# Performance work log

Measured on AMD Instinct MI355X. Metric: run time of the kernel, lower is better.

Reference implementation:

```python
import jax, jax.numpy as jnp
import numpy as np

DIM = 256
NUM_HEADS = 4
HEAD_DIM = DIM // NUM_HEADS
SCALE = HEAD_DIM ** -0.5


def setup_inputs() -> dict:
    key = jax.random.key(0)
    k1, k2, k3, k4 = jax.random.split(key, 4)
    B, N, C = 2, 4096, DIM
    x = jax.random.normal(k1, (B, N, C), dtype=jnp.float32)
    # nn.Linear(dim, 3*dim, bias=False): weight [3C, C], y = x @ W.T
    w_qkv = jax.random.normal(k2, (3 * C, C), dtype=jnp.float32) * (C ** -0.5)
    # nn.Linear(dim, dim) with bias
    w_proj = jax.random.normal(k3, (C, C), dtype=jnp.float32) * (C ** -0.5)
    b_proj = jax.random.normal(k4, (C,), dtype=jnp.float32) * 0.02
    return {"x": x, "w_qkv": w_qkv, "w_proj": w_proj, "b_proj": b_proj}


def reference(x, w_qkv, w_proj, b_proj):
    B, N, C = x.shape
    H, D = NUM_HEADS, HEAD_DIM
    qkv = x @ w_qkv.T                                  # [B, N, 3C]
    qkv = qkv.reshape(B, N, 3, H, D).transpose(2, 0, 3, 1, 4)  # [3, B, H, N, D]
    q, k, v = qkv[0], qkv[1], qkv[2]
    attn = jnp.einsum("bhnd,bhmd->bhnm", q, k) * SCALE  # [B, H, N, N]
    attn = jax.nn.softmax(attn, axis=-1)
    out = jnp.einsum("bhnm,bhmd->bhnd", attn, v)        # [B, H, N, D]
    out = out.transpose(0, 2, 1, 3).reshape(B, N, C)
    out = out @ w_proj.T + b_proj
    return out
```

## Files before the change

kernel.cpp:

```cpp
#include <hip/hip_runtime.h>
#include <hip/hip_bf16.h>
#include <stdint.h>

typedef __bf16 bf16;
typedef __bf16 bf16x8 __attribute__((ext_vector_type(8)));
typedef __bf16 bf16x4 __attribute__((ext_vector_type(4)));
typedef float  f32x4  __attribute__((ext_vector_type(4)));

#define MFMA16(a, b, c) __builtin_amdgcn_mfma_f32_16x16x32_bf16((a), (b), (c), 0, 0, 0)

#define BB   2
#define NN   4096
#define CC   256
#define HH   4
#define DD   64
#define BH   8
#define SL2E 0.1803368801111244f

__device__ __forceinline__ void gload_lds16(const void* g, void* l) {
    __builtin_amdgcn_global_load_lds(
        (const __attribute__((address_space(1))) void*)g,
        (__attribute__((address_space(3))) void*)l, 16, 0, 0);
}

__global__ __launch_bounds__(256) void cvt_all(const float* __restrict__ x,
                                               const float* __restrict__ wq,
                                               const float* __restrict__ wp,
                                               bf16* __restrict__ xb,
                                               bf16* __restrict__ wqb,
                                               bf16* __restrict__ wpb) {
    int i = blockIdx.x * 256 + threadIdx.x;
    const float* src; bf16* dst; int j;
    if (i < 524288)      { src = x;  dst = xb;  j = i; }
    else if (i < 573440) { src = wq; dst = wqb; j = i - 524288; }
    else if (i < 589824) { src = wp; dst = wpb; j = i - 573440; }
    else return;
    f32x4 v = ((const f32x4*)src)[j];
    bf16x4 o;
    o[0] = (bf16)v[0]; o[1] = (bf16)v[1]; o[2] = (bf16)v[2]; o[3] = (bf16)v[3];
    ((bf16x4*)dst)[j] = o;
}

__global__ __launch_bounds__(256) void gemm_qkv(const bf16* __restrict__ X,
                                                const bf16* __restrict__ W,
                                                bf16* __restrict__ Q,
                                                bf16* __restrict__ K,
                                                bf16* __restrict__ Vt) {
    const int wave = threadIdx.x >> 6;
    const int lane = threadIdx.x & 63;
    const int lr = lane & 15;
    const int lg = lane >> 4;
    const int row0 = blockIdx.x * 128 + wave * 32;
    const int col0 = blockIdx.y * 64;

    f32x4 acc[2][4] = {};
    for (int k0 = 0; k0 < 256; k0 += 32) {
        bf16x8 a[2], b[4];
#pragma unroll
        for (int i = 0; i < 2; i++)
            a[i] = *(const bf16x8*)&X[(size_t)(row0 + 16 * i + lr) * 256 + k0 + 8 * lg];
#pragma unroll
        for (int t = 0; t < 4; t++)
            b[t] = *(const bf16x8*)&W[(size_t)(col0 + 16 * t + lr) * 256 + k0 + 8 * lg];
#pragma unroll
        for (int i = 0; i < 2; i++)
#pragma unroll
            for (int t = 0; t < 4; t++)
                acc[i][t] = MFMA16(a[i], b[t], acc[i][t]);
    }

    const int s = col0 >> 8;
    const int h = (col0 >> 6) & 3;
    if (s == 2) {
#pragma unroll
        for (int i = 0; i < 2; i++) {
#pragma unroll
            for (int t = 0; t < 4; t++) {
                int row = row0 + 16 * i + 4 * lg;
                int d   = 16 * t + lr;
                int bh  = ((row >> 12) << 2) | h;
                int nb  = row & 4095;
                int g   = nb >> 5, m = (nb >> 2) & 7;
                int np  = (g << 5) + ((m & 3) << 3) + ((m >> 2) << 2);
                bf16x4 o4;
#pragma unroll
                for (int r = 0; r < 4; r++) o4[r] = (bf16)acc[i][t][r];
                *(bf16x4*)&Vt[((size_t)bh * DD + d) * NN + np] = o4;
            }
        }
    } else {
        bf16* dst = (s == 0) ? Q : K;
        const float sc = (s == 0) ? SL2E : 1.0f;
#pragma unroll
        for (int i = 0; i < 2; i++) {
#pragma unroll
            for (int t = 0; t < 4; t++) {
#pragma unroll
                for (int r = 0; r < 4; r++) {
                    int row = row0 + 16 * i + 4 * lg + r;
                    int d   = 16 * t + lr;
                    int bh  = ((row >> 12) << 2) | h;
                    int n   = row & 4095;
                    dst[((size_t)bh * NN + n) * DD + d] = (bf16)(acc[i][t][r] * sc);
                }
            }
        }
    }
}

template<int NSPLIT>
__global__ __launch_bounds__(256, 2) void flash_attn(const bf16* __restrict__ Q,
                                                     const bf16* __restrict__ K,
                                                     const bf16* __restrict__ Vt,
                                                     bf16* __restrict__ Op,
                                                     float* __restrict__ ps) {
    __shared__ __align__(16) char kv_lds[2][16384];

    const int id  = blockIdx.x + 16 * (blockIdx.y + 8 * blockIdx.z);
    constexpr int CHUNK = 16 * NSPLIT;
    const int nid = (id & 7) * CHUNK + (id >> 3);
    const int qx  = nid & 15;
    const int g   = nid >> 4;
    const int bh  = g & 7;
    const int zid = g >> 3;

    const int wave = threadIdx.x >> 6;
    const int lane = threadIdx.x & 63;
    const int lr   = lane & 15;
    const int lg   = lane >> 4;
    const int tid  = threadIdx.x;
    const int swz  = (lr & 7) << 4;

    const char* Khb  = (const char*)(K  + (size_t)bh * NN * DD);
    const char* Vthb = (const char*)(Vt + (size_t)bh * DD * NN);
    const bf16* Qh   = Q + (size_t)bh * NN * DD;

    const int qw = qx * 256 + wave * 64;

    bf16x8 qf[4][2];
#pragma unroll
    for (int s = 0; s < 4; s++) {
        qf[s][0] = *(const bf16x8*)&Qh[(size_t)(qw + 16 * s + lr) * DD + 8 * lg];
        qf[s][1] = *(const bf16x8*)&Qh[(size_t)(qw + 16 * s + lr) * DD + 32 + 8 * lg];
    }

    const int L  = tid * 16;
    const int r0 = L >> 7;
    const int c0 = (L & 127) ^ ((r0 & 7) << 4);

    bf16x8 onesf;
#pragma unroll
    for (int j = 0; j < 8; j++) onesf[j] = (bf16)1.0f;

    f32x4 oa[4][4] = {};
    f32x4 psacc[4] = {};

    auto stage = [&](int t, char* buf) {
        const int kv0 = t * 64;
        gload_lds16(Khb + (size_t)(kv0 + r0) * 128 + c0,             buf + L);
        gload_lds16(Khb + (size_t)(kv0 + r0 + 32) * 128 + c0,        buf + 4096 + L);
        gload_lds16(Vthb + (size_t)r0 * 8192 + kv0 * 2 + c0,         buf + 8192 + L);
        gload_lds16(Vthb + (size_t)(r0 + 32) * 8192 + kv0 * 2 + c0,  buf + 12288 + L);
    };

    auto compute = [&](const char* buf) {
        const char* kb = buf;
        const char* vb = buf + 8192;

        bf16x8 pb[4][2];
        __builtin_amdgcn_s_setprio(1);
#pragma unroll
        for (int t = 0; t < 4; t++) {
            const char* rowk = kb + (16 * t + lr) * 128;
            bf16x8 kf0 = *(const bf16x8*)(rowk + ((16 * lg) ^ swz));
            bf16x8 kf1 = *(const bf16x8*)(rowk + ((64 + 16 * lg) ^ swz));
#pragma unroll
            for (int s = 0; s < 4; s++) {
                f32x4 z = {0.f, 0.f, 0.f, 0.f};
                z = MFMA16(kf0, qf[s][0], z);
                z = MFMA16(kf1, qf[s][1], z);
#pragma unroll
                for (int r = 0; r < 4; r++)
                    pb[s][t >> 1][4 * (t & 1) + r] = (bf16)__builtin_exp2f(z[r]);
            }
        }
        __builtin_amdgcn_s_setprio(0);

        bf16x8 vf[2][4];
#pragma unroll
        for (int dt = 0; dt < 4; dt++) {
            const char* rowv = vb + (16 * dt + lr) * 128;
            vf[0][dt] = *(const bf16x8*)(rowv + ((16 * lg) ^ swz));
            vf[1][dt] = *(const bf16x8*)(rowv + ((64 + 16 * lg) ^ swz));
        }

        __builtin_amdgcn_s_setprio(1);
#pragma unroll
        for (int s = 0; s < 4; s++) {
#pragma unroll
            for (int dt = 0; dt < 4; dt++) {
                oa[s][dt] = MFMA16(vf[0][dt], pb[s][0], oa[s][dt]);
                oa[s][dt] = MFMA16(vf[1][dt], pb[s][1], oa[s][dt]);
            }
            psacc[s] = MFMA16(onesf, pb[s][0], psacc[s]);
            psacc[s] = MFMA16(onesf, pb[s][1], psacc[s]);
        }
        __builtin_amdgcn_s_setprio(0);
    };

    constexpr int nt = 64 / NSPLIT;
    const int t0 = zid * nt;

    char* cur = &kv_lds[0][0];
    char* nxt = &kv_lds[1][0];

    stage(t0, cur);
    stage(t0 + 1, nxt);

    for (int t = 0; t < nt; t++) {
        if (t + 1 < nt) asm volatile("s_waitcnt vmcnt(4)" ::: "memory");
        else            asm volatile("s_waitcnt vmcnt(0)" ::: "memory");
        __builtin_amdgcn_s_barrier();
        compute(cur);
        asm volatile("" ::: "memory");
        __builtin_amdgcn_s_barrier();
        if (t + 2 < nt) stage(t0 + t + 2, cur);
        char* tmp = cur; cur = nxt; nxt = tmp;
    }

    const int b = bh >> 2, hd = bh & 3;
#pragma unroll
    for (int s = 0; s < 4; s++) {
        const int q = qw + 16 * s + lr;
        bf16* Oz = Op + (size_t)zid * 8192 * 256
                      + ((size_t)b * NN + q) * CC + hd * 64;
#pragma unroll
        for (int dt = 0; dt < 4; dt++) {
            bf16x4 o4;
#pragma unroll
            for (int i = 0; i < 4; i++) o4[i] = (bf16)oa[s][dt][i];
            *(bf16x4*)&Oz[16 * dt + 4 * lg] = o4;
        }
        ps[((size_t)zid * BH + bh) * NN + q] = psacc[s][0];
    }
}

template<int NSPLIT>
__global__ __launch_bounds__(256) void gemm_proj(const bf16* __restrict__ Op,
                                                 const float* __restrict__ ps,
                                                 const bf16* __restrict__ W,
                                                 const float* __restrict__ bias,
                                                 float* __restrict__ Out) {
    const int wave = threadIdx.x >> 6;
    const int lane = threadIdx.x & 63;
    const int lr = lane & 15;
    const int lg = lane >> 4;
    const int row0 = blockIdx.x * 128 + wave * 32;
    const int col0 = blockIdx.y * 64;

    float rinv[2][4];
#pragma unroll
    for (int i = 0; i < 2; i++) {
        int row = row0 + 16 * i + lr;
        int n = row & 4095, b = row >> 12;
#pragma unroll
        for (int h = 0; h < 4; h++) {
            float s0 = 0.0f;
#pragma unroll
            for (int z = 0; z < NSPLIT; z++)
                s0 += ps[((size_t)z * BH + b * 4 + h) * NN + n];
            rinv[i][h] = 1.0f / s0;
        }
    }

    f32x4 acc[2][4] = {};
    for (int k0 = 0; k0 < 256; k0 += 32) {
        const int h = k0 >> 6;
        bf16x8 a[2], b4[4];
#pragma unroll
        for (int i = 0; i < 2; i++) {
            size_t base = (size_t)(row0 + 16 * i + lr) * 256 + k0 + 8 * lg;
            float av[8] = {};
#pragma unroll
            for (int z = 0; z < NSPLIT; z++) {
                bf16x8 u = *(const bf16x8*)&Op[base + (size_t)z * 8192 * 256];
#pragma unroll
                for (int j = 0; j < 8; j++) av[j] += (float)u[j];
            }
            const float rv = rinv[i][h];
#pragma unroll
            for (int j = 0; j < 8; j++) a[i][j] = (bf16)(av[j] * rv);
        }
#pragma unroll
        for (int t = 0; t < 4; t++)
            b4[t] = *(const bf16x8*)&W[(size_t)(col0 + 16 * t + lr) * 256 + k0 + 8 * lg];
#pragma unroll
        for (int i = 0; i < 2; i++)
#pragma unroll
            for (int t = 0; t < 4; t++)
                acc[i][t] = MFMA16(a[i], b4[t], acc[i][t]);
    }
#pragma unroll
    for (int t = 0; t < 4; t++) {
        float bv = bias[col0 + 16 * t + lr];
#pragma unroll
        for (int i = 0; i < 2; i++) {
#pragma unroll
            for (int r = 0; r < 4; r++) {
                int row = row0 + 16 * i + 4 * lg + r;
                Out[(size_t)row * 256 + col0 + 16 * t + lr] = acc[i][t][r] + bv;
            }
        }
    }
}

extern "C" void kernel_launch(void* const* d_in, const int* in_sizes, int n_in,
                              void* d_out, int out_size, void* d_ws, size_t ws_size,
                              hipStream_t stream) {
    const float* x      = (const float*)d_in[0];
    const float* w_qkv  = (const float*)d_in[1];
    const float* w_proj = (const float*)d_in[2];
    const float* b_proj = (const float*)d_in[3];
    float* out = (float*)d_out;

    char* ws = (char*)d_ws;
    size_t off = 0;
    auto alloc = [&](size_t bytes) { void* p = ws + off; off += (bytes + 255) & ~(size_t)255; return p; };

    bf16* xb  = (bf16*)alloc((size_t)8192 * 256 * 2);
    bf16* wqb = (bf16*)alloc((size_t)768 * 256 * 2);
    bf16* wpb = (bf16*)alloc((size_t)256 * 256 * 2);
    bf16* Qb  = (bf16*)alloc((size_t)BH * NN * DD * 2);
    bf16* Kb  = (bf16*)alloc((size_t)BH * NN * DD * 2);
    bf16* Vtb = (bf16*)alloc((size_t)BH * NN * DD * 2);

    const size_t opBytes = (size_t)8192 * 256 * 2;
    const size_t psBytes = (size_t)BH * NN * 4;
    const size_t perSplit = ((opBytes + 255) & ~(size_t)255) + ((psBytes + 255) & ~(size_t)255);
    const size_t rem = (ws_size > off) ? (ws_size - off) : 0;
    const int nsplit = (rem >= 4 * perSplit) ? 4 : ((rem >= 2 * perSplit) ? 2 : 1);

    bf16*  Op = (bf16*)alloc(opBytes * nsplit);
    float* ps = (float*)alloc(psBytes * nsplit);

    cvt_all<<<2304, 256, 0, stream>>>(x, w_qkv, w_proj, xb, wqb, wpb);
    gemm_qkv<<<dim3(64, 12), 256, 0, stream>>>(xb, wqb, Qb, Kb, Vtb);
    if (nsplit == 4) {
        flash_attn<4><<<dim3(16, 8, 4), 256, 0, stream>>>(Qb, Kb, Vtb, Op, ps);
        gemm_proj<4><<<dim3(64, 4), 256, 0, stream>>>(Op, ps, wpb, b_proj, out);
    } else if (nsplit == 2) {
        flash_attn<2><<<dim3(16, 8, 2), 256, 0, stream>>>(Qb, Kb, Vtb, Op, ps);
        gemm_proj<2><<<dim3(64, 4), 256, 0, stream>>>(Op, ps, wpb, b_proj, out);
    } else {
        flash_attn<1><<<dim3(16, 8, 1), 256, 0, stream>>>(Qb, Kb, Vtb, Op, ps);
        gemm_proj<1><<<dim3(64, 4), 256, 0, stream>>>(Op, ps, wpb, b_proj, out);
    }
}
```

Before: 101.0 us.

## Replace LDS-staged K/V pipeline with direct global loads in single-wave blocks

```diff
diff --git a/kernel.cpp b/kernel.cpp
--- a/kernel.cpp
+++ b/kernel.cpp
@@ -16,12 +16,6 @@
 #define DD   64
 #define BH   8
 #define SL2E 0.1803368801111244f
-
-__device__ __forceinline__ void gload_lds16(const void* g, void* l) {
-    __builtin_amdgcn_global_load_lds(
-        (const __attribute__((address_space(1))) void*)g,
-        (__attribute__((address_space(3))) void*)l, 16, 0, 0);
-}
 
 __global__ __launch_bounds__(256) void cvt_all(const float* __restrict__ x,
                                                const float* __restrict__ wq,
@@ -109,33 +103,29 @@
 }
 
 template<int NSPLIT>
-__global__ __launch_bounds__(256, 2) void flash_attn(const bf16* __restrict__ Q,
-                                                     const bf16* __restrict__ K,
-                                                     const bf16* __restrict__ Vt,
-                                                     bf16* __restrict__ Op,
-                                                     float* __restrict__ ps) {
-    __shared__ __align__(16) char kv_lds[2][16384];
-
-    const int id  = blockIdx.x + 16 * (blockIdx.y + 8 * blockIdx.z);
-    constexpr int CHUNK = 16 * NSPLIT;
+__global__ __launch_bounds__(64, 2) void flash_attn(const bf16* __restrict__ Q,
+                                                    const bf16* __restrict__ K,
+                                                    const bf16* __restrict__ Vt,
+                                                    bf16* __restrict__ Op,
+                                                    float* __restrict__ ps) {
+    constexpr int TOTAL = 64 * 8 * NSPLIT;
+    constexpr int CHUNK = TOTAL / 8;
+    const int id  = blockIdx.x + 64 * (blockIdx.y + 8 * blockIdx.z);
     const int nid = (id & 7) * CHUNK + (id >> 3);
-    const int qx  = nid & 15;
-    const int g   = nid >> 4;
+    const int qx  = nid & 63;
+    const int g   = nid >> 6;
     const int bh  = g & 7;
     const int zid = g >> 3;
 
-    const int wave = threadIdx.x >> 6;
     const int lane = threadIdx.x & 63;
     const int lr   = lane & 15;
     const int lg   = lane >> 4;
-    const int tid  = threadIdx.x;
-    const int swz  = (lr & 7) << 4;
 
     const char* Khb  = (const char*)(K  + (size_t)bh * NN * DD);
     const char* Vthb = (const char*)(Vt + (size_t)bh * DD * NN);
     const bf16* Qh   = Q + (size_t)bh * NN * DD;
 
-    const int qw = qx * 256 + wave * 64;
+    const int qw = qx * 64;
 
     bf16x8 qf[4][2];
 #pragma unroll
@@ -144,10 +134,6 @@
         qf[s][1] = *(const bf16x8*)&Qh[(size_t)(qw + 16 * s + lr) * DD + 32 + 8 * lg];
     }
 
-    const int L  = tid * 16;
-    const int r0 = L >> 7;
-    const int c0 = (L & 127) ^ ((r0 & 7) << 4);
-
     bf16x8 onesf;
 #pragma unroll
     for (int j = 0; j < 8; j++) onesf[j] = (bf16)1.0f;
@@ -155,77 +141,51 @@
     f32x4 oa[4][4] = {};
     f32x4 psacc[4] = {};
 
-    auto stage = [&](int t, char* buf) {
-        const int kv0 = t * 64;
-        gload_lds16(Khb + (size_t)(kv0 + r0) * 128 + c0,             buf + L);
-        gload_lds16(Khb + (size_t)(kv0 + r0 + 32) * 128 + c0,        buf + 4096 + L);
-        gload_lds16(Vthb + (size_t)r0 * 8192 + kv0 * 2 + c0,         buf + 8192 + L);
-        gload_lds16(Vthb + (size_t)(r0 + 32) * 8192 + kv0 * 2 + c0,  buf + 12288 + L);
-    };
-
-    auto compute = [&](const char* buf) {
-        const char* kb = buf;
-        const char* vb = buf + 8192;
+    constexpr int nt = 64 / NSPLIT;
+    const int tb = zid * nt;
+
+    for (int t = 0; t < nt; t++) {
+        const int kv0 = (tb + t) * 64;
+
+        bf16x8 kf0[4], kf1[4];
+#pragma unroll
+        for (int u = 0; u < 4; u++) {
+            const char* rowk = Khb + (size_t)(kv0 + 16 * u + lr) * 128;
+            kf0[u] = *(const bf16x8*)(rowk + 16 * lg);
+            kf1[u] = *(const bf16x8*)(rowk + 64 + 16 * lg);
+        }
+        bf16x8 vf0[4], vf1[4];
+#pragma unroll
+        for (int dt = 0; dt < 4; dt++) {
+            const char* rowv = Vthb + (size_t)(16 * dt + lr) * 8192 + (size_t)kv0 * 2;
+            vf0[dt] = *(const bf16x8*)(rowv + 16 * lg);
+            vf1[dt] = *(const bf16x8*)(rowv + 64 + 16 * lg);
+        }
 
         bf16x8 pb[4][2];
-        __builtin_amdgcn_s_setprio(1);
-#pragma unroll
-        for (int t = 0; t < 4; t++) {
-            const char* rowk = kb + (16 * t + lr) * 128;
-            bf16x8 kf0 = *(const bf16x8*)(rowk + ((16 * lg) ^ swz));
-            bf16x8 kf1 = *(const bf16x8*)(rowk + ((64 + 16 * lg) ^ swz));
+#pragma unroll
+        for (int u = 0; u < 4; u++) {
 #pragma unroll
             for (int s = 0; s < 4; s++) {
                 f32x4 z = {0.f, 0.f, 0.f, 0.f};
-                z = MFMA16(kf0, qf[s][0], z);
-                z = MFMA16(kf1, qf[s][1], z);
+                z = MFMA16(kf0[u], qf[s][0], z);
+                z = MFMA16(kf1[u], qf[s][1], z);
 #pragma unroll
                 for (int r = 0; r < 4; r++)
-                    pb[s][t >> 1][4 * (t & 1) + r] = (bf16)__builtin_exp2f(z[r]);
-            }
-        }
-        __builtin_amdgcn_s_setprio(0);
-
-        bf16x8 vf[2][4];
-#pragma unroll
-        for (int dt = 0; dt < 4; dt++) {
-            const char* rowv = vb + (16 * dt + lr) * 128;
-            vf[0][dt] = *(const bf16x8*)(rowv + ((16 * lg) ^ swz));
-            vf[1][dt] = *(const bf16x8*)(rowv + ((64 + 16 * lg) ^ swz));
-        }
-
-        __builtin_amdgcn_s_setprio(1);
+                    pb[s][u >> 1][4 * (u & 1) + r] = (bf16)__builtin_exp2f(z[r]);
+            }
+        }
+
 #pragma unroll
         for (int s = 0; s < 4; s++) {
 #pragma unroll
             for (int dt = 0; dt < 4; dt++) {
-                oa[s][dt] = MFMA16(vf[0][dt], pb[s][0], oa[s][dt]);
-                oa[s][dt] = MFMA16(vf[1][dt], pb[s][1], oa[s][dt]);
+                oa[s][dt] = MFMA16(vf0[dt], pb[s][0], oa[s][dt]);
+                oa[s][dt] = MFMA16(vf1[dt], pb[s][1], oa[s][dt]);
             }
             psacc[s] = MFMA16(onesf, pb[s][0], psacc[s]);
             psacc[s] = MFMA16(onesf, pb[s][1], psacc[s]);
         }
-        __builtin_amdgcn_s_setprio(0);
-    };
-
-    constexpr int nt = 64 / NSPLIT;
-    const int t0 = zid * nt;
-
-    char* cur = &kv_lds[0][0];
-    char* nxt = &kv_lds[1][0];
-
-    stage(t0, cur);
-    stage(t0 + 1, nxt);
-
-    for (int t = 0; t < nt; t++) {
-        if (t + 1 < nt) asm volatile("s_waitcnt vmcnt(4)" ::: "memory");
-        else            asm volatile("s_waitcnt vmcnt(0)" ::: "memory");
-        __builtin_amdgcn_s_barrier();
-        compute(cur);
-        asm volatile("" ::: "memory");
-        __builtin_amdgcn_s_barrier();
-        if (t + 2 < nt) stage(t0 + t + 2, cur);
-        char* tmp = cur; cur = nxt; nxt = tmp;
     }
 
     const int b = bh >> 2, hd = bh & 3;
@@ -346,13 +306,13 @@
     cvt_all<<<2304, 256, 0, stream>>>(x, w_qkv, w_proj, xb, wqb, wpb);
     gemm_qkv<<<dim3(64, 12), 256, 0, stream>>>(xb, wqb, Qb, Kb, Vtb);
     if (nsplit == 4) {
-        flash_attn<4><<<dim3(16, 8, 4), 256, 0, stream>>>(Qb, Kb, Vtb, Op, ps);
+        flash_attn<4><<<dim3(64, 8, 4), 64, 0, stream>>>(Qb, Kb, Vtb, Op, ps);
         gemm_proj<4><<<dim3(64, 4), 256, 0, stream>>>(Op, ps, wpb, b_proj, out);
     } else if (nsplit == 2) {
-        flash_attn<2><<<dim3(16, 8, 2), 256, 0, stream>>>(Qb, Kb, Vtb, Op, ps);
+        flash_attn<2><<<dim3(64, 8, 2), 64, 0, stream>>>(Qb, Kb, Vtb, Op, ps);
         gemm_proj<2><<<dim3(64, 4), 256, 0, stream>>>(Op, ps, wpb, b_proj, out);
     } else {
-        flash_attn<1><<<dim3(16, 8, 1), 256, 0, stream>>>(Qb, Kb, Vtb, Op, ps);
+        flash_attn<1><<<dim3(64, 8, 1), 64, 0, stream>>>(Qb, Kb, Vtb, Op, ps);
         gemm_proj<1><<<dim3(64, 4), 256, 0, stream>>>(Op, ps, wpb, b_proj, out);
     }
 }
```

Result: slower. 116.8 us (+15.6%).

## Use two waves per flash block, each handling 128 query rows

Applied to the files above, without the earlier changes.

```diff
diff --git a/kernel.cpp b/kernel.cpp
--- a/kernel.cpp
+++ b/kernel.cpp
@@ -109,15 +109,16 @@
 }
 
 template<int NSPLIT>
-__global__ __launch_bounds__(256, 2) void flash_attn(const bf16* __restrict__ Q,
+__global__ __launch_bounds__(128, 2) void flash_attn(const bf16* __restrict__ Q,
                                                      const bf16* __restrict__ K,
                                                      const bf16* __restrict__ Vt,
                                                      bf16* __restrict__ Op,
                                                      float* __restrict__ ps) {
     __shared__ __align__(16) char kv_lds[2][16384];
 
+    constexpr int TOTAL = 16 * 8 * NSPLIT;
+    constexpr int CHUNK = TOTAL / 8;
     const int id  = blockIdx.x + 16 * (blockIdx.y + 8 * blockIdx.z);
-    constexpr int CHUNK = 16 * NSPLIT;
     const int nid = (id & 7) * CHUNK + (id >> 3);
     const int qx  = nid & 15;
     const int g   = nid >> 4;
@@ -135,73 +136,73 @@
     const char* Vthb = (const char*)(Vt + (size_t)bh * DD * NN);
     const bf16* Qh   = Q + (size_t)bh * NN * DD;
 
-    const int qw = qx * 256 + wave * 64;
-
-    bf16x8 qf[4][2];
-#pragma unroll
-    for (int s = 0; s < 4; s++) {
+    const int qw = qx * 256 + wave * 128;
+
+    bf16x8 qf[8][2];
+#pragma unroll
+    for (int s = 0; s < 8; s++) {
         qf[s][0] = *(const bf16x8*)&Qh[(size_t)(qw + 16 * s + lr) * DD + 8 * lg];
         qf[s][1] = *(const bf16x8*)&Qh[(size_t)(qw + 16 * s + lr) * DD + 32 + 8 * lg];
     }
 
-    const int L  = tid * 16;
-    const int r0 = L >> 7;
-    const int c0 = (L & 127) ^ ((r0 & 7) << 4);
+    const int L = tid * 16;
 
     bf16x8 onesf;
 #pragma unroll
     for (int j = 0; j < 8; j++) onesf[j] = (bf16)1.0f;
 
-    f32x4 oa[4][4] = {};
-    f32x4 psacc[4] = {};
+    f32x4 oa[8][4] = {};
+    f32x4 psacc[8] = {};
 
     auto stage = [&](int t, char* buf) {
         const int kv0 = t * 64;
-        gload_lds16(Khb + (size_t)(kv0 + r0) * 128 + c0,             buf + L);
-        gload_lds16(Khb + (size_t)(kv0 + r0 + 32) * 128 + c0,        buf + 4096 + L);
-        gload_lds16(Vthb + (size_t)r0 * 8192 + kv0 * 2 + c0,         buf + 8192 + L);
-        gload_lds16(Vthb + (size_t)(r0 + 32) * 8192 + kv0 * 2 + c0,  buf + 12288 + L);
+#pragma unroll
+        for (int p = 0; p < 4; p++) {
+            const int idx = p * 2048 + L;
+            const int rr  = idx >> 7;
+            const int cc  = (idx & 127) ^ ((rr & 7) << 4);
+            gload_lds16(Khb + (size_t)(kv0 + rr) * 128 + cc,        buf + idx);
+            gload_lds16(Vthb + (size_t)rr * 8192 + kv0 * 2 + cc,    buf + 8192 + idx);
+        }
     };
 
     auto compute = [&](const char* buf) {
         const char* kb = buf;
         const char* vb = buf + 8192;
 
-        bf16x8 pb[4][2];
+        bf16x8 pb[8][2];
         __builtin_amdgcn_s_setprio(1);
 #pragma unroll
-        for (int t = 0; t < 4; t++) {
-            const char* rowk = kb + (16 * t + lr) * 128;
+        for (int u = 0; u < 4; u++) {
+            const char* rowk = kb + (16 * u + lr) * 128;
             bf16x8 kf0 = *(const bf16x8*)(rowk + ((16 * lg) ^ swz));
             bf16x8 kf1 = *(const bf16x8*)(rowk + ((64 + 16 * lg) ^ swz));
 #pragma unroll
-            for (int s = 0; s < 4; s++) {
+            for (int s = 0; s < 8; s++) {
                 f32x4 z = {0.f, 0.f, 0.f, 0.f};
                 z = MFMA16(kf0, qf[s][0], z);
                 z = MFMA16(kf1, qf[s][1], z);
 #pragma unroll
                 for (int r = 0; r < 4; r++)
-                    pb[s][t >> 1][4 * (t & 1) + r] = (bf16)__builtin_exp2f(z[r]);
+                    pb[s][u >> 1][4 * (u & 1) + r] = (bf16)__builtin_exp2f(z[r]);
             }
         }
         __builtin_amdgcn_s_setprio(0);
 
-        bf16x8 vf[2][4];
+        __builtin_amdgcn_s_setprio(1);
 #pragma unroll
         for (int dt = 0; dt < 4; dt++) {
             const char* rowv = vb + (16 * dt + lr) * 128;
-            vf[0][dt] = *(const bf16x8*)(rowv + ((16 * lg) ^ swz));
-            vf[1][dt] = *(const bf16x8*)(rowv + ((64 + 16 * lg) ^ swz));
-        }
-
-        __builtin_amdgcn_s_setprio(1);
-#pragma unroll
-        for (int s = 0; s < 4; s++) {
-#pragma unroll
-            for (int dt = 0; dt < 4; dt++) {
-                oa[s][dt] = MFMA16(vf[0][dt], pb[s][0], oa[s][dt]);
-                oa[s][dt] = MFMA16(vf[1][dt], pb[s][1], oa[s][dt]);
-            }
+            bf16x8 vf0 = *(const bf16x8*)(rowv + ((16 * lg) ^ swz));
+            bf16x8 vf1 = *(const bf16x8*)(rowv + ((64 + 16 * lg) ^ swz));
+#pragma unroll
+            for (int s = 0; s < 8; s++) {
+                oa[s][dt] = MFMA16(vf0, pb[s][0], oa[s][dt]);
+                oa[s][dt] = MFMA16(vf1, pb[s][1], oa[s][dt]);
+            }
+        }
+#pragma unroll
+        for (int s = 0; s < 8; s++) {
             psacc[s] = MFMA16(onesf, pb[s][0], psacc[s]);
             psacc[s] = MFMA16(onesf, pb[s][1], psacc[s]);
         }
@@ -218,7 +219,7 @@
     stage(t0 + 1, nxt);
 
     for (int t = 0; t < nt; t++) {
-        if (t + 1 < nt) asm volatile("s_waitcnt vmcnt(4)" ::: "memory");
+        if (t + 1 < nt) asm volatile("s_waitcnt vmcnt(8)" ::: "memory");
         else            asm volatile("s_waitcnt vmcnt(0)" ::: "memory");
         __builtin_amdgcn_s_barrier();
         compute(cur);
@@ -230,7 +231,7 @@
 
     const int b = bh >> 2, hd = bh & 3;
 #pragma unroll
-    for (int s = 0; s < 4; s++) {
+    for (int s = 0; s < 8; s++) {
         const int q = qw + 16 * s + lr;
         bf16* Oz = Op + (size_t)zid * 8192 * 256
                       + ((size_t)b * NN + q) * CC + hd * 64;
@@ -346,13 +347,13 @@
     cvt_all<<<2304, 256, 0, stream>>>(x, w_qkv, w_proj, xb, wqb, wpb);
     gemm_qkv<<<dim3(64, 12), 256, 0, stream>>>(xb, wqb, Qb, Kb, Vtb);
     if (nsplit == 4) {
-        flash_attn<4><<<dim3(16, 8, 4), 256, 0, stream>>>(Qb, Kb, Vtb, Op, ps);
+        flash_attn<4><<<dim3(16, 8, 4), 128, 0, stream>>>(Qb, Kb, Vtb, Op, ps);
         gemm_proj<4><<<dim3(64, 4), 256, 0, stream>>>(Op, ps, wpb, b_proj, out);
     } else if (nsplit == 2) {
-        flash_attn<2><<<dim3(16, 8, 2), 256, 0, stream>>>(Qb, Kb, Vtb, Op, ps);
+        flash_attn<2><<<dim3(16, 8, 2), 128, 0, stream>>>(Qb, Kb, Vtb, Op, ps);
         gemm_proj<2><<<dim3(64, 4), 256, 0, stream>>>(Op, ps, wpb, b_proj, out);
     } else {
-        flash_attn<1><<<dim3(16, 8, 1), 256, 0, stream>>>(Qb, Kb, Vtb, Op, ps);
+        flash_attn<1><<<dim3(16, 8, 1), 128, 0, stream>>>(Qb, Kb, Vtb, Op, ps);
         gemm_proj<1><<<dim3(64, 4), 256, 0, stream>>>(Op, ps, wpb, b_proj, out);
     }
 }
```

Result: slower. 191.7 us (+89.8%).
